# Performance work log

Hardware: AMD Instinct MI355X
Metric: run time of the kernel (lower is better)

## Reference

```python
import jax, jax.numpy as jnp
import numpy as np


def setup_inputs() -> dict:
    key = jax.random.key(0)
    ks = jax.random.split(key, 9)
    N, C, H, W, K = 8, 512, 64, 64, 32
    C4 = C // 4
    s = lambda k, shape, scale=0.02: jax.random.normal(k, shape, dtype=jnp.float32) * scale
    return {
        "x": jax.random.normal(ks[0], (N, C, H, W), dtype=jnp.float32),
        "y": jax.random.normal(ks[1], (N, K, C), dtype=jnp.float32),
        "wq": s(ks[2], (C4, C)),
        "bq": s(ks[3], (C4,)),
        "wk": s(ks[4], (C4, C)),
        "bk": s(ks[5], (C4,)),
        "wv": s(ks[6], (C, C)),
        "bv": s(ks[7], (C,)),
        "scale": s(ks[8], (1,), 1.0),
    }


def reference(x, y, wq, bq, wk, bk, wv, bv, scale):
    N, C, H, W = x.shape
    # 1x1 conv query: (N,C,H,W) -> (N,C4,H,W) -> (N, HW, C4)
    q = jnp.einsum('nchw,oc->nhwo', x, wq) + bq  # (N,H,W,C4)
    q = q.reshape(N, H * W, -1)                   # (N, HW, C4)
    # key/value linears on centers y: (N,K,C)
    k = y @ wk.T + bk                             # (N, K, C4)
    v = y @ wv.T + bv                             # (N, K, C)
    energy = jnp.einsum('npc,nkc->npk', q, k)     # (N, HW, K)
    attn = jax.nn.softmax(energy, axis=-1)
    out = jnp.einsum('nkc,npk->ncp', v, attn)     # (N, C, HW)
    out = out.reshape(N, C, H, W)
    return scale[0] * out + x
```

## Files before the change

kernel.cpp:

```cpp
#include <hip/hip_runtime.h>


#define N_  8
#define C_  512
#define HW_ 4096
#define K_  32

typedef __attribute__((ext_vector_type(8))) short bf16x8;
typedef __attribute__((ext_vector_type(4))) float f32x4;
typedef __attribute__((ext_vector_type(4))) unsigned short u16x4;
typedef __attribute__((ext_vector_type(2))) int i32x2;
typedef __attribute__((ext_vector_type(4))) int i32x4;

__device__ __forceinline__ unsigned short f2b(float f) {
    union { float f; unsigned u; } v; v.f = f;
    unsigned r = v.u + 0x7FFFu + ((v.u >> 16) & 1u);
    return (unsigned short)(r >> 16);
}
__device__ __forceinline__ float b2f(unsigned short h) {
    union { unsigned u; float f; } v; v.u = ((unsigned)h) << 16; return v.f;
}

__device__ __forceinline__ int wqk_idx(int kk, int c) {
    return ((((c >> 5) * 2 + (kk >> 4)) * 64 + ((c >> 3) & 3) * 16 + (kk & 15)) << 3) + (c & 7);
}

__global__ __launch_bounds__(256) void prep_kernel(
    const float* __restrict__ y, const float* __restrict__ wq, const float* __restrict__ bq,
    const float* __restrict__ wk, const float* __restrict__ bk,
    const float* __restrict__ wv, const float* __restrict__ bv,
    unsigned short* __restrict__ wqkf, float* __restrict__ bqk, unsigned short* __restrict__ vtf)
{
    const int bid = blockIdx.x;
    const int t = threadIdx.x;

    if (bid < 256) {
        __shared__ float vred[3][4][16][8];
        const int n   = bid >> 5;
        const int ct  = bid & 31;
        const int cl  = t & 15;
        const int kko = (t >> 4) & 3;
        const int jq4 = t >> 6;
        const int c   = ct * 16 + cl;

        const float* yb  = y  + ((size_t)n * K_ + kko * 8) * C_ + jq4 * 128;
        const float* wvb = wv + (size_t)c * C_ + jq4 * 128;
        float acc[8] = {0,0,0,0,0,0,0,0};
        #pragma unroll 4
        for (int jj = 0; jj < 32; ++jj) {
            float4 w4 = *(const float4*)(wvb + jj * 4);
            #pragma unroll
            for (int u = 0; u < 8; ++u) {
                float4 y4 = *(const float4*)(yb + (size_t)u * C_ + jj * 4);
                acc[u] += y4.x * w4.x + y4.y * w4.y + y4.z * w4.z + y4.w * w4.w;
            }
        }
        if (jq4 > 0) {
            #pragma unroll
            for (int u = 0; u < 8; ++u) vred[jq4 - 1][kko][cl][u] = acc[u];
        }
        __syncthreads();
        if (jq4 == 0) {
            const float bvc = bv[c];
            unsigned short o[8];
            #pragma unroll
            for (int u = 0; u < 8; ++u) {
                float s = acc[u] + vred[0][kko][cl][u] + vred[1][kko][cl][u]
                        + vred[2][kko][cl][u] + bvc;
                o[u] = f2b(s);
            }
            i32x4 pk = { (int)(o[0] | ((unsigned)o[1] << 16)), (int)(o[2] | ((unsigned)o[3] << 16)),
                         (int)(o[4] | ((unsigned)o[5] << 16)), (int)(o[6] | ((unsigned)o[7] << 16)) };
            *(i32x4*)(vtf + (size_t)n * (K_ * C_) + (size_t)((ct * 64 + kko * 16 + cl) * 8)) = pk;
        }
    } else {
        __shared__ __align__(16) float kp[2][128];
        __shared__ __align__(16) float kr[128];
        const int b = bid - 256;
        const int n = b >> 5, kk = b & 31;
        const int o = t & 127, half = t >> 7;

        const float* yb  = y  + ((size_t)n * K_ + kk) * C_ + half * 256;
        const float* wkb = wk + (size_t)o * C_ + half * 256;
        float a = 0.f;
        #pragma unroll 4
        for (int jq = 0; jq < 64; ++jq) {
            float4 w4 = *(const float4*)(wkb + jq * 4);
            float4 y4 = *(const float4*)(yb + jq * 4);
            a += y4.x * w4.x + y4.y * w4.y + y4.z * w4.z + y4.w * w4.w;
        }
        kp[half][o] = a;
        __syncthreads();
        if (t < 128) kr[t] = kp[0][t] + kp[1][t] + bk[t];
        __syncthreads();
        if (t < 64) {
            float s = kr[t] * bq[t] + kr[t + 64] * bq[t + 64];
            #pragma unroll
            for (int d = 32; d > 0; d >>= 1) s += __shfl_down(s, d);
            if (t == 0) bqk[n * K_ + kk] = s;
        }
        const int c1 = t, c2 = t + 256;
        float s1 = 0.f, s2 = 0.f;
        for (int oq = 0; oq < 32; ++oq) {
            float4 k4 = *(const float4*)(&kr[oq * 4]);
            const float* wq0 = wq + (size_t)(oq * 4) * C_;
            s1 += k4.x * wq0[c1] + k4.y * wq0[C_ + c1] + k4.z * wq0[2*C_ + c1] + k4.w * wq0[3*C_ + c1];
            s2 += k4.x * wq0[c2] + k4.y * wq0[C_ + c2] + k4.z * wq0[2*C_ + c2] + k4.w * wq0[3*C_ + c2];
        }
        unsigned short* wqf_n = wqkf + (size_t)n * (K_ * C_);
        wqf_n[wqk_idx(kk, c1)] = f2b(s1);
        wqf_n[wqk_idx(kk, c2)] = f2b(s2);
    }
}

__global__ __launch_bounds__(256) void main_kernel(
    const float* __restrict__ x, const unsigned short* __restrict__ wqkf,
    const unsigned short* __restrict__ vtf, const float* __restrict__ bqk,
    const float* __restrict__ scale, float* __restrict__ out)
{
    __shared__ __align__(16) unsigned short xl[16384];
    __shared__ float e_lds[32][33];

    const int bid = (blockIdx.x & 7) * 128 + (blockIdx.x >> 3);
    const int n  = bid >> 7;
    const int p0 = (bid & 127) * 32;
    const int t  = threadIdx.x;
    const int w  = t >> 6, l = t & 63;
    const int l15 = l & 15, lg = l >> 4;
    const float* xg = x + (size_t)n * C_ * HW_;
    float* og = out + (size_t)n * C_ * HW_;
    const unsigned short* wqf  = wqkf + (size_t)n * (K_ * C_);
    const unsigned short* vtfn = vtf  + (size_t)n * (K_ * C_);

    const int mh = w;
    const int kt = w >> 1;
    bf16x8 vf[8];
    #pragma unroll
    for (int mi = 0; mi < 8; ++mi)
        vf[mi] = *(const bf16x8*)(vtfn + ((size_t)(mh * 8 + mi) * 64 + l) * 8);
    bf16x8 b0 = *(const bf16x8*)(wqf + ((size_t)(0 * 2 + kt) * 64 + l) * 8);
    bf16x8 b1 = *(const bf16x8*)(wqf + ((size_t)(1 * 2 + kt) * 64 + l) * 8);

    {
        const int px = t & 31, g = t >> 5;
        const float* xc = xg + p0 + px;
        float ra[8], rb[8];
        #pragma unroll
        for (int j = 0; j < 8; ++j) ra[j] = xc[(size_t)(g * 8 + j) * HW_];
        for (int u = 0; u < 8; ++u) {
            if (u < 7) {
                #pragma unroll
                for (int j = 0; j < 8; ++j)
                    rb[j] = xc[(size_t)(g * 8 + (u + 1) * 64 + j) * HW_];
            }
            unsigned short o[8];
            #pragma unroll
            for (int j = 0; j < 8; ++j) o[j] = f2b(ra[j]);
            const int cbase = g * 8 + u * 64;
            const int elem = ((cbase >> 5) * 1024) + (((cbase >> 3) & 3) * 256) + px * 8;
            i32x4 pk = { (int)(o[0] | ((unsigned)o[1] << 16)), (int)(o[2] | ((unsigned)o[3] << 16)),
                         (int)(o[4] | ((unsigned)o[5] << 16)), (int)(o[6] | ((unsigned)o[7] << 16)) };
            *(i32x4*)(xl + elem) = pk;
            #pragma unroll
            for (int j = 0; j < 8; ++j) ra[j] = rb[j];
        }
    }
    __syncthreads();

    {
        const int pt = w & 1;
        const unsigned short* xbase = xl + lg * 256 + (pt * 16 + l15) * 8;
        f32x4 acc = {0.f, 0.f, 0.f, 0.f};
        for (int cs = 0; cs < 16; ++cs) {
            bf16x8 b2;
            if (cs < 14) b2 = *(const bf16x8*)(wqf + ((size_t)((cs + 2) * 2 + kt) * 64 + l) * 8);
            const bf16x8 af = *(const bf16x8*)(xbase + cs * 1024);
            acc = __builtin_amdgcn_mfma_f32_16x16x32_bf16(af, b0, acc, 0, 0, 0);
            b0 = b1; b1 = b2;
        }
        const float bq_ = bqk[n * K_ + kt * 16 + l15];
        #pragma unroll
        for (int r = 0; r < 4; ++r)
            e_lds[pt * 16 + lg * 4 + r][kt * 16 + l15] = acc[r] + bq_;
    }
    __syncthreads();

    bf16x8 paf0, paf1;
    {
        const float* er0 = e_lds[l15];
        const float* er1 = e_lds[16 + l15];
        float e0[32], e1[32];
        #pragma unroll
        for (int k = 0; k < 32; ++k) { e0[k] = er0[k]; e1[k] = er1[k]; }
        float m0 = e0[0], m1 = e1[0];
        #pragma unroll
        for (int k = 1; k < 32; ++k) { m0 = fmaxf(m0, e0[k]); m1 = fmaxf(m1, e1[k]); }
        float s0 = 0.f, s1 = 0.f;
        #pragma unroll
        for (int k = 0; k < 32; ++k) {
            e0[k] = __expf(e0[k] - m0); s0 += e0[k];
            e1[k] = __expf(e1[k] - m1); s1 += e1[k];
        }
        const float i0 = 1.f / s0, i1 = 1.f / s1;
        #pragma unroll
        for (int j = 0; j < 8; ++j) {
            paf0[j] = (short)f2b(e0[8 * lg + j] * i0);
            paf1[j] = (short)f2b(e1[8 * lg + j] * i1);
        }
    }

    {
        const float fs = scale[0];
        const int pxa = p0 + l15, pxb = p0 + 16 + l15;
        const int mt0 = mh * 8;

        #pragma unroll
        for (int mi = 0; mi < 8; ++mi) {
            const int mt = mt0 + mi;
            f32x4 d0 = __builtin_amdgcn_mfma_f32_16x16x32_bf16(vf[mi], paf0, (f32x4){0.f,0.f,0.f,0.f}, 0, 0, 0);
            f32x4 d1 = __builtin_amdgcn_mfma_f32_16x16x32_bf16(vf[mi], paf1, (f32x4){0.f,0.f,0.f,0.f}, 0, 0, 0);
            const int base = (mt >> 1) * 1024 + ((2 * mt + (lg >> 1)) & 3) * 256 + (lg & 1) * 4;
            const u16x4 ra = *(const u16x4*)(xl + base + l15 * 8);
            const u16x4 rb = *(const u16x4*)(xl + base + (16 + l15) * 8);
            const int cc = mt * 16 + lg * 4;
            #pragma unroll
            for (int r = 0; r < 4; ++r) {
                og[(size_t)(cc + r) * HW_ + pxa] = fs * d0[r] + b2f(ra[r]);
                og[(size_t)(cc + r) * HW_ + pxb] = fs * d1[r] + b2f(rb[r]);
            }
        }
    }
}

extern "C" void kernel_launch(void* const* d_in, const int* in_sizes, int n_in,
                              void* d_out, int out_size, void* d_ws, size_t ws_size,
                              hipStream_t stream) {
    const float* x     = (const float*)d_in[0];
    const float* y     = (const float*)d_in[1];
    const float* wq    = (const float*)d_in[2];
    const float* bq    = (const float*)d_in[3];
    const float* wk    = (const float*)d_in[4];
    const float* bk    = (const float*)d_in[5];
    const float* wv    = (const float*)d_in[6];
    const float* bv    = (const float*)d_in[7];
    const float* scale = (const float*)d_in[8];

    unsigned short* wqkf = (unsigned short*)d_ws;
    unsigned short* vtf  = wqkf + (size_t)N_ * K_ * C_;
    float* bqk = (float*)((char*)d_ws + 524288);

    prep_kernel<<<512, 256, 0, stream>>>(y, wq, bq, wk, bk, wv, bv, wqkf, bqk, vtf);
    main_kernel<<<1024, 256, 0, stream>>>(x, wqkf, vtf, bqk, scale, (float*)d_out);
}
```

Measured before the change: 58.60 us.

## Split x staging into two halves overlapped with query MFMAs; use hardware bf16 pack

The fp32-to-bf16 staging of the x tile into LDS is split into two halves. The first half's query-energy MFMAs run while the second half's global loads are in flight, which overlaps HBM latency with matrix work at the cost of an extra barrier and more live registers. Software bf16 rounding is replaced with the v_cvt_pk_bf16_f32 instruction. The energy LDS row is padded to 36 floats so the softmax stage can read it with float4 loads.

```diff
diff --git a/kernel.cpp b/kernel.cpp
--- a/kernel.cpp
+++ b/kernel.cpp
@@ -9,7 +9,6 @@
 typedef __attribute__((ext_vector_type(8))) short bf16x8;
 typedef __attribute__((ext_vector_type(4))) float f32x4;
 typedef __attribute__((ext_vector_type(4))) unsigned short u16x4;
-typedef __attribute__((ext_vector_type(2))) int i32x2;
 typedef __attribute__((ext_vector_type(4))) int i32x4;
 
 __device__ __forceinline__ unsigned short f2b(float f) {
@@ -19,6 +18,11 @@
 }
 __device__ __forceinline__ float b2f(unsigned short h) {
     union { unsigned u; float f; } v; v.u = ((unsigned)h) << 16; return v.f;
+}
+__device__ __forceinline__ int cvtpk(float a, float b) {
+    int r;
+    asm("v_cvt_pk_bf16_f32 %0, %1, %2" : "=v"(r) : "v"(a), "v"(b));
+    return r;
 }
 
 __device__ __forceinline__ int wqk_idx(int kk, int c) {
@@ -119,7 +123,7 @@
     const float* __restrict__ scale, float* __restrict__ out)
 {
     __shared__ __align__(16) unsigned short xl[16384];
-    __shared__ float e_lds[32][33];
+    __shared__ float e_lds[32][36];
 
     const int bid = (blockIdx.x & 7) * 128 + (blockIdx.x >> 3);
     const int n  = bid >> 7;
@@ -141,37 +145,58 @@
     bf16x8 b0 = *(const bf16x8*)(wqf + ((size_t)(0 * 2 + kt) * 64 + l) * 8);
     bf16x8 b1 = *(const bf16x8*)(wqf + ((size_t)(1 * 2 + kt) * 64 + l) * 8);
 
-    {
-        const int px = t & 31, g = t >> 5;
-        const float* xc = xg + p0 + px;
-        float ra[8], rb[8];
-        #pragma unroll
-        for (int j = 0; j < 8; ++j) ra[j] = xc[(size_t)(g * 8 + j) * HW_];
-        for (int u = 0; u < 8; ++u) {
-            if (u < 7) {
-                #pragma unroll
-                for (int j = 0; j < 8; ++j)
-                    rb[j] = xc[(size_t)(g * 8 + (u + 1) * 64 + j) * HW_];
-            }
-            unsigned short o[8];
-            #pragma unroll
-            for (int j = 0; j < 8; ++j) o[j] = f2b(ra[j]);
+    const int px = t & 31, g = t >> 5;
+    const float* xc = xg + p0 + px;
+    const int pt = w & 1;
+    f32x4 acc = {0.f, 0.f, 0.f, 0.f};
+    const unsigned short* xbase = xl + lg * 256 + (pt * 16 + l15) * 8;
+
+    {
+        float r0[4][8];
+        #pragma unroll
+        for (int u = 0; u < 4; ++u)
+            #pragma unroll
+            for (int j = 0; j < 8; ++j)
+                r0[u][j] = xc[(size_t)(g * 8 + u * 64 + j) * HW_];
+        #pragma unroll
+        for (int u = 0; u < 4; ++u) {
             const int cbase = g * 8 + u * 64;
             const int elem = ((cbase >> 5) * 1024) + (((cbase >> 3) & 3) * 256) + px * 8;
-            i32x4 pk = { (int)(o[0] | ((unsigned)o[1] << 16)), (int)(o[2] | ((unsigned)o[3] << 16)),
-                         (int)(o[4] | ((unsigned)o[5] << 16)), (int)(o[6] | ((unsigned)o[7] << 16)) };
+            i32x4 pk = { cvtpk(r0[u][0], r0[u][1]), cvtpk(r0[u][2], r0[u][3]),
+                         cvtpk(r0[u][4], r0[u][5]), cvtpk(r0[u][6], r0[u][7]) };
             *(i32x4*)(xl + elem) = pk;
-            #pragma unroll
-            for (int j = 0; j < 8; ++j) ra[j] = rb[j];
         }
     }
     __syncthreads();
 
     {
-        const int pt = w & 1;
-        const unsigned short* xbase = xl + lg * 256 + (pt * 16 + l15) * 8;
-        f32x4 acc = {0.f, 0.f, 0.f, 0.f};
-        for (int cs = 0; cs < 16; ++cs) {
+        float r1[4][8];
+        #pragma unroll
+        for (int u = 0; u < 4; ++u)
+            #pragma unroll
+            for (int j = 0; j < 8; ++j)
+                r1[u][j] = xc[(size_t)(g * 8 + (u + 4) * 64 + j) * HW_];
+
+        for (int cs = 0; cs < 8; ++cs) {
+            bf16x8 b2 = *(const bf16x8*)(wqf + ((size_t)((cs + 2) * 2 + kt) * 64 + l) * 8);
+            const bf16x8 af = *(const bf16x8*)(xbase + cs * 1024);
+            acc = __builtin_amdgcn_mfma_f32_16x16x32_bf16(af, b0, acc, 0, 0, 0);
+            b0 = b1; b1 = b2;
+        }
+
+        #pragma unroll
+        for (int u = 0; u < 4; ++u) {
+            const int cbase = g * 8 + (u + 4) * 64;
+            const int elem = ((cbase >> 5) * 1024) + (((cbase >> 3) & 3) * 256) + px * 8;
+            i32x4 pk = { cvtpk(r1[u][0], r1[u][1]), cvtpk(r1[u][2], r1[u][3]),
+                         cvtpk(r1[u][4], r1[u][5]), cvtpk(r1[u][6], r1[u][7]) };
+            *(i32x4*)(xl + elem) = pk;
+        }
+    }
+    __syncthreads();
+
+    {
+        for (int cs = 8; cs < 16; ++cs) {
             bf16x8 b2;
             if (cs < 14) b2 = *(const bf16x8*)(wqf + ((size_t)((cs + 2) * 2 + kt) * 64 + l) * 8);
             const bf16x8 af = *(const bf16x8*)(xbase + cs * 1024);
@@ -187,11 +212,14 @@
 
     bf16x8 paf0, paf1;
     {
-        const float* er0 = e_lds[l15];
-        const float* er1 = e_lds[16 + l15];
         float e0[32], e1[32];
         #pragma unroll
-        for (int k = 0; k < 32; ++k) { e0[k] = er0[k]; e1[k] = er1[k]; }
+        for (int i = 0; i < 8; ++i) {
+            float4 q0 = *(const float4*)&e_lds[l15][4 * i];
+            float4 q1 = *(const float4*)&e_lds[16 + l15][4 * i];
+            e0[4*i] = q0.x; e0[4*i+1] = q0.y; e0[4*i+2] = q0.z; e0[4*i+3] = q0.w;
+            e1[4*i] = q1.x; e1[4*i+1] = q1.y; e1[4*i+2] = q1.z; e1[4*i+3] = q1.w;
+        }
         float m0 = e0[0], m1 = e1[0];
         #pragma unroll
         for (int k = 1; k < 32; ++k) { m0 = fmaxf(m0, e0[k]); m1 = fmaxf(m1, e1[k]); }
@@ -202,11 +230,13 @@
             e1[k] = __expf(e1[k] - m1); s1 += e1[k];
         }
         const float i0 = 1.f / s0, i1 = 1.f / s1;
-        #pragma unroll
-        for (int j = 0; j < 8; ++j) {
-            paf0[j] = (short)f2b(e0[8 * lg + j] * i0);
-            paf1[j] = (short)f2b(e1[8 * lg + j] * i1);
-        }
+        union { int i[4]; bf16x8 v; } u0, u1;
+        #pragma unroll
+        for (int jj = 0; jj < 4; ++jj) {
+            u0.i[jj] = cvtpk(e0[8*lg + 2*jj] * i0, e0[8*lg + 2*jj + 1] * i0);
+            u1.i[jj] = cvtpk(e1[8*lg + 2*jj] * i1, e1[8*lg + 2*jj + 1] * i1);
+        }
+        paf0 = u0.v; paf1 = u1.v;
     }
 
     {
```

Result: faster. 54.70 us, median of 2 (-6.7%).
